# Kernel optimization log

Hardware: AMD Instinct MI355X
Metric: run time of the kernel (lower is better)

Reference implementation:

```python
import jax, jax.numpy as jnp
import numpy as np


def setup_inputs() -> dict:
    key = jax.random.key(0)
    k1, k2, k3, k4 = jax.random.split(key, 4)
    B, T, F, U = 64, 1024, 256, 512
    x = jax.random.normal(k1, (B, T, F), dtype=jnp.float32)
    # small init scale keeps the linear-activation cell state numerically tame
    kernel = jax.random.normal(k2, (F, 4 * U), dtype=jnp.float32) * 0.05
    recurrent_kernel = jax.random.normal(k3, (U, 4 * U), dtype=jnp.float32) * 0.05
    bias = jax.random.normal(k4, (4 * U,), dtype=jnp.float32) * 0.05
    return {"x": x, "kernel": kernel, "recurrent_kernel": recurrent_kernel, "bias": bias}


def reference(x, kernel, recurrent_kernel, bias):
    # Keras LSTM with activation=None (linear candidate / linear output),
    # recurrent_activation=sigmoid, gate order [i, f, c, o]; then external tanh.
    B, T, F = x.shape
    U = recurrent_kernel.shape[0]
    # precompute input projections for all timesteps: [T, B, 4U]
    xz = jnp.einsum('btf,fg->tbg', x, kernel) + bias

    def step(carry, xz_t):
        h, c = carry
        z = xz_t + h @ recurrent_kernel  # [B, 4U]
        i, f, g, o = jnp.split(z, 4, axis=-1)
        i = jax.nn.sigmoid(i)
        f = jax.nn.sigmoid(f)
        o = jax.nn.sigmoid(o)
        c = f * c + i * g          # candidate activation is linear (None)
        h = o * c                  # output activation is linear (None)
        return (h, c), h

    h0 = jnp.zeros((B, U), dtype=x.dtype)
    c0 = jnp.zeros((B, U), dtype=x.dtype)
    (_, _), hs = jax.lax.scan(step, (h0, c0), xz)  # hs: [T, B, U]
    seq = jnp.swapaxes(hs, 0, 1)  # [B, T, U] (return_sequences=True)
    return jnp.tanh(seq)          # external activation applied post-hoc
```

## Files before the change

### kernel.cpp

```cpp
#include <hip/hip_runtime.h>
#include <stdint.h>


#define Tt   1024
#define Uu   512
#define G4U  2048
#define NWG  256
#define NTHR 128
#define TAGSTRIDE 16

#define WF_ELEMS (2 * 24 * 64 * 8)
#define WF_BYTES (WF_ELEMS * 2)
#define ZB_PLANE (16 * 17)
#define ZB_HALF  (4 * ZB_PLANE)
#define SMEM_BYTES (WF_BYTES + 2 * ZB_HALF * 4)

typedef short  bf16x8 __attribute__((ext_vector_type(8)));
typedef float  f32x4  __attribute__((ext_vector_type(4)));
typedef int    int4v  __attribute__((ext_vector_type(4)));
typedef unsigned int u32;

__device__ __forceinline__ unsigned short f2bf(float f) {
  u32 u = __builtin_bit_cast(u32, f);
  u += 0x7fffu + ((u >> 16) & 1u);
  return (unsigned short)(u >> 16);
}
__device__ __forceinline__ u32 umin32(u32 a, u32 b) { return a < b ? a : b; }

__device__ __forceinline__ int4v ld16_ag(const u32* p) {
  int4v r;
  asm volatile("global_load_dwordx4 %0, %1, off sc1"
               : "=v"(r) : "v"(p) : "memory");
  return r;
}
__device__ __forceinline__ int4v ld16_nc(const float* p) {
  int4v r;
  asm volatile("global_load_dwordx4 %0, %1, off"
               : "=v"(r) : "v"(p) : "memory");
  return r;
}
__device__ __forceinline__ void store4_ag(u32* p, u32 v) {
  asm volatile("global_store_dword %0, %1, off sc1"
               :: "v"(p), "v"(v) : "memory");
}

__device__ __forceinline__ float sigf(float z) {
  return __builtin_amdgcn_rcpf(1.f + __expf(-z));
}
__device__ __forceinline__ float tanh_fast(float v) {
  const float e = __expf(-2.f * fabsf(v));
  const float r = (1.f - e) * __builtin_amdgcn_rcpf(1.f + e);
  return copysignf(r, v);
}

extern "C" __global__ void __launch_bounds__(NTHR, 1)
lstm_persistent(const float* __restrict__ x,
                const float* __restrict__ Wk,
                const float* __restrict__ Rk,
                const float* __restrict__ bias,
                float* __restrict__ out,
                u32* __restrict__ hbuf,
                u32* __restrict__ tags)
{
  extern __shared__ char smem[];
  unsigned short* wf   = (unsigned short*)smem;
  float*          zbuf = (float*)(smem + WF_BYTES);

  const int bid = blockIdx.x;
  const int tid = threadIdx.x;
  const int w   = tid >> 6;
  const int l   = tid & 63;
  const int g   = bid & 3;
  const int m   = bid >> 2;

  for (int i = tid; i < WF_ELEMS; i += NTHR) {
    const int j    = i & 7;
    const int lane = (i >> 3) & 63;
    const int kt   = (i >> 9) % 24;
    const int nt   = (i >> 9) / 24;
    const int k    = kt * 32 + ((lane >> 4) << 3) + j;
    const int n    = nt * 16 + (lane & 15);
    const int zc   = (n >> 3) * Uu + m * 8 + (n & 7);
    const float v  = (k < 256) ? Wk[(size_t)k * G4U + zc]
                               : Rk[(size_t)(k - 256) * G4U + zc];
    wf[i] = f2bf(v);
  }
  __syncthreads();

  bf16x8 wfx[4][2];
  #pragma unroll
  for (int q = 0; q < 4; ++q)
    #pragma unroll
    for (int nt = 0; nt < 2; ++nt)
      wfx[q][nt] = *(const bf16x8*)(wf + (((nt * 24) + (2 * q + w)) * 64 + l) * 8);

  const int row_c = tid >> 3;
  const int uu    = tid & 7;
  const int b_out = g * 16 + row_c;
  const int u_out = m * 8 + uu;
  float breg[4];
  #pragma unroll
  for (int gg = 0; gg < 4; ++gg) breg[gg] = bias[gg * Uu + u_out];
  float creg = 0.f;

  const int b_ld = g * 16 + (l & 15);
  const int kq   = (l >> 4) * 8;
  const u32* tagp = tags + ((size_t)g * 64 + l) * TAGSTRIDE;

  int4v xv[4][2];
  {
    const float* xp0 = x + ((size_t)b_ld * Tt + 0) * 256 + kq;
    #pragma unroll
    for (int q = 0; q < 4; ++q) {
      const int kt = 2 * q + w;
      xv[q][0] = ld16_nc(xp0 + kt * 32);
      xv[q][1] = ld16_nc(xp0 + kt * 32 + 4);
    }
  }
  u32 tv = 0;
  if (w == 0)
    asm volatile("global_load_dword %0, %1, off sc1"
                 : "=v"(tv) : "v"(tagp) : "memory");
  asm volatile("s_waitcnt vmcnt(0)" ::: "memory");
  __builtin_amdgcn_sched_barrier(0);

  for (int t = 0; t < Tt; ++t) {
    f32x4 aX0 = {0.f, 0.f, 0.f, 0.f};
    f32x4 aX1 = {0.f, 0.f, 0.f, 0.f};
    #pragma unroll
    for (int q = 0; q < 4; ++q) {
      const f32x4 v0 = __builtin_bit_cast(f32x4, xv[q][0]);
      const f32x4 v1 = __builtin_bit_cast(f32x4, xv[q][1]);
      int r0, r1, r2, r3;
      asm("v_cvt_pk_bf16_f32 %0, %1, %2" : "=v"(r0) : "v"(v0[0]), "v"(v0[1]));
      asm("v_cvt_pk_bf16_f32 %0, %1, %2" : "=v"(r1) : "v"(v0[2]), "v"(v0[3]));
      asm("v_cvt_pk_bf16_f32 %0, %1, %2" : "=v"(r2) : "v"(v1[0]), "v"(v1[1]));
      asm("v_cvt_pk_bf16_f32 %0, %1, %2" : "=v"(r3) : "v"(v1[2]), "v"(v1[3]));
      const int4v ai = {r0, r1, r2, r3};
      const bf16x8 a = __builtin_bit_cast(bf16x8, ai);
      aX0 = __builtin_amdgcn_mfma_f32_16x16x32_bf16(a, wfx[q][0], aX0, 0, 0, 0);
      aX1 = __builtin_amdgcn_mfma_f32_16x16x32_bf16(a, wfx[q][1], aX1, 0, 0, 0);
    }

    if (w == 0) {
      asm volatile("s_waitcnt vmcnt(1)" ::: "memory");
      __builtin_amdgcn_sched_barrier(0);
      while (!__all(tv >= (u32)t)) {
        __builtin_amdgcn_s_sleep(1);
        asm volatile("global_load_dword %0, %1, off sc1\n\ts_waitcnt vmcnt(0)"
                     : "=v"(tv) : "v"(tagp) : "memory");
        __builtin_amdgcn_sched_barrier(0);
      }
    }
    __builtin_amdgcn_s_barrier();
    __builtin_amdgcn_sched_barrier(0);

    const u32* hp = hbuf + ((size_t)(t & 1) * 64 + b_ld) * Uu + kq;
    int4v hf[16];
    #pragma unroll
    for (int q = 0; q < 8; ++q) {
      hf[2 * q]     = ld16_ag(hp + (2 * q + w) * 32);
      hf[2 * q + 1] = ld16_ag(hp + (2 * q + w) * 32 + 4);
    }
    {
      const int tn = (t + 1 < Tt) ? t + 1 : t;
      const float* xpn = x + ((size_t)b_ld * Tt + tn) * 256 + kq;
      #pragma unroll
      for (int q = 0; q < 4; ++q) {
        const int kt = 2 * q + w;
        xv[q][0] = ld16_nc(xpn + kt * 32);
        xv[q][1] = ld16_nc(xpn + kt * 32 + 4);
      }
    }

    asm volatile("s_waitcnt vmcnt(8)" ::: "memory");
    __builtin_amdgcn_sched_barrier(0);
    for (;;) {
      u32 m0 = ~0u, m1 = ~0u, m2 = ~0u, m3 = ~0u;
      #pragma unroll
      for (int q = 0; q < 16; ++q) {
        m0 = umin32(m0, (u32)hf[q][0]);
        m1 = umin32(m1, (u32)hf[q][1]);
        m2 = umin32(m2, (u32)hf[q][2]);
        m3 = umin32(m3, (u32)hf[q][3]);
      }
      const u32 mv = umin32(umin32(m0, m1), umin32(m2, m3));
      if (__all((mv >> 16) == (u32)t)) break;
      __builtin_amdgcn_s_sleep(1);
      #pragma unroll
      for (int q = 0; q < 8; ++q) {
        hf[2 * q]     = ld16_ag(hp + (2 * q + w) * 32);
        hf[2 * q + 1] = ld16_ag(hp + (2 * q + w) * 32 + 4);
      }
      asm volatile("s_waitcnt vmcnt(0)" ::: "memory");
      __builtin_amdgcn_sched_barrier(0);
    }

    f32x4 aH0 = {0.f, 0.f, 0.f, 0.f};
    f32x4 aH1 = {0.f, 0.f, 0.f, 0.f};
    #pragma unroll
    for (int q = 0; q < 8; ++q) {
      const int kt = 8 + 2 * q + w;
      const u32 w0_ = __builtin_amdgcn_perm((u32)hf[2*q][1],   (u32)hf[2*q][0],   0x05040100u);
      const u32 w1_ = __builtin_amdgcn_perm((u32)hf[2*q][3],   (u32)hf[2*q][2],   0x05040100u);
      const u32 w2_ = __builtin_amdgcn_perm((u32)hf[2*q+1][1], (u32)hf[2*q+1][0], 0x05040100u);
      const u32 w3_ = __builtin_amdgcn_perm((u32)hf[2*q+1][3], (u32)hf[2*q+1][2], 0x05040100u);
      const int4v ai = {(int)w0_, (int)w1_, (int)w2_, (int)w3_};
      const bf16x8 a = __builtin_bit_cast(bf16x8, ai);
      const bf16x8 b0 = *(const bf16x8*)(wf + ((0 * 24 + kt) * 64 + l) * 8);
      const bf16x8 b1 = *(const bf16x8*)(wf + ((1 * 24 + kt) * 64 + l) * 8);
      aH0 = __builtin_amdgcn_mfma_f32_16x16x32_bf16(a, b0, aH0, 0, 0, 0);
      aH1 = __builtin_amdgcn_mfma_f32_16x16x32_bf16(a, b1, aH1, 0, 0, 0);
    }

    const f32x4 z0 = aX0 + aH0;
    const f32x4 z1 = aX1 + aH1;

    float* zb = zbuf + (t & 1) * ZB_HALF;
    {
      float* zw = zb + ((w * 2 + 0) * 16 + (l >> 4) * 4) * 17 + (l & 15);
      #pragma unroll
      for (int r = 0; r < 4; ++r) {
        zw[r * 17]           = z0[r];
        zw[r * 17 + 16 * 17] = z1[r];
      }
    }
    __syncthreads();

    float z[4];
    #pragma unroll
    for (int gg = 0; gg < 4; ++gg) {
      const int n  = gg * 8 + uu;
      const int nt = n >> 4, nc = n & 15;
      z[gg] = zb[((0 + nt) * 16 + row_c) * 17 + nc]
            + zb[((2 + nt) * 16 + row_c) * 17 + nc]
            + breg[gg];
    }
    const float ig = sigf(z[0]);
    const float fg = sigf(z[1]);
    const float og = sigf(z[3]);
    const float cc = fg * creg + ig * z[2];
    creg = cc;
    const float hh = og * cc;

    asm volatile("s_waitcnt vmcnt(0)" ::: "memory");
    __builtin_amdgcn_sched_barrier(0);
    const u32 hw = ((u32)(t + 1) << 16) | (u32)f2bf(hh);
    store4_ag(hbuf + ((size_t)((t + 1) & 1) * 64 + b_out) * Uu + u_out, hw);
    __builtin_amdgcn_s_barrier();
    __builtin_amdgcn_sched_barrier(0);
    if (tid == 0)
      store4_ag(tags + ((size_t)g * 64 + m) * TAGSTRIDE, (u32)(t + 1));
    if (w == 0)
      asm volatile("global_load_dword %0, %1, off sc1"
                   : "=v"(tv) : "v"(tagp) : "memory");
    {
      const float ov = tanh_fast(hh);
      float* op = out + ((size_t)b_out * Tt + t) * Uu + u_out;
      asm volatile("global_store_dword %0, %1, off nt"
                   :: "v"(op), "v"(ov) : "memory");
    }
  }
}

extern "C" void kernel_launch(void* const* d_in, const int* in_sizes, int n_in,
                              void* d_out, int out_size, void* d_ws, size_t ws_size,
                              hipStream_t stream) {
  const float* x    = (const float*)d_in[0];
  const float* Wk   = (const float*)d_in[1];
  const float* Rk   = (const float*)d_in[2];
  const float* bias = (const float*)d_in[3];
  float* out = (float*)d_out;
  u32* hbuf = (u32*)d_ws;
  u32* tags = (u32*)((char*)d_ws + (size_t)2 * 64 * Uu * sizeof(u32));

  (void)hipMemsetAsync(d_ws, 0,
                       (size_t)2 * 64 * Uu * sizeof(u32)
                         + (size_t)4 * 64 * TAGSTRIDE * sizeof(u32),
                       stream);

  (void)hipFuncSetAttribute((const void*)lstm_persistent,
                            hipFuncAttributeMaxDynamicSharedMemorySize,
                            SMEM_BYTES);

  hipLaunchKernelGGL(lstm_persistent, dim3(NWG), dim3(NTHR), SMEM_BYTES, stream,
                     x, Wk, Rk, bias, out, hbuf, tags);
}
```

Before: 3.174 ms.

## Speculatively prefetch next-step h before polling tags, drop per-step tag barrier

Instead of waiting on a per-group tag flag and a workgroup barrier before loading the recurrent state, each step now issues the h loads for the next timestep right after publishing its own output. It then validates them via the timestamp embedded in each packed element. Tag polling only happens on the slow path when the speculative data is stale, which removes a serial tag round-trip and a barrier from the critical path. The risk is extra reload traffic when the data is stale, plus reliance on vmcnt ordering: a wait of 17 outstanding operations followed by a wait of 1 with the output store in flight.

```diff
diff --git a/kernel.cpp b/kernel.cpp
--- a/kernel.cpp
+++ b/kernel.cpp
@@ -42,6 +42,12 @@
 __device__ __forceinline__ void store4_ag(u32* p, u32 v) {
   asm volatile("global_store_dword %0, %1, off sc1"
                :: "v"(p), "v"(v) : "memory");
+}
+__device__ __forceinline__ u32 load_tag_wait(const u32* p) {
+  u32 r;
+  asm volatile("global_load_dword %0, %1, off sc1\n\ts_waitcnt vmcnt(0)"
+               : "=v"(r) : "v"(p) : "memory");
+  return r;
 }
 
 __device__ __forceinline__ float sigf(float z) {
@@ -108,6 +114,7 @@
   const u32* tagp = tags + ((size_t)g * 64 + l) * TAGSTRIDE;
 
   int4v xv[4][2];
+  int4v hf[16];
   {
     const float* xp0 = x + ((size_t)b_ld * Tt + 0) * 256 + kq;
     #pragma unroll
@@ -116,15 +123,20 @@
       xv[q][0] = ld16_nc(xp0 + kt * 32);
       xv[q][1] = ld16_nc(xp0 + kt * 32 + 4);
     }
+    const u32* hp0 = hbuf + (size_t)b_ld * Uu + kq;
+    #pragma unroll
+    for (int q = 0; q < 8; ++q) {
+      hf[2 * q]     = ld16_ag(hp0 + (2 * q + w) * 32);
+      hf[2 * q + 1] = ld16_ag(hp0 + (2 * q + w) * 32 + 4);
+    }
   }
-  u32 tv = 0;
-  if (w == 0)
-    asm volatile("global_load_dword %0, %1, off sc1"
-                 : "=v"(tv) : "v"(tagp) : "memory");
   asm volatile("s_waitcnt vmcnt(0)" ::: "memory");
   __builtin_amdgcn_sched_barrier(0);
 
   for (int t = 0; t < Tt; ++t) {
+    asm volatile("s_waitcnt vmcnt(17)" ::: "memory");
+    __builtin_amdgcn_sched_barrier(0);
+
     f32x4 aX0 = {0.f, 0.f, 0.f, 0.f};
     f32x4 aX1 = {0.f, 0.f, 0.f, 0.f};
     #pragma unroll
@@ -142,39 +154,9 @@
       aX1 = __builtin_amdgcn_mfma_f32_16x16x32_bf16(a, wfx[q][1], aX1, 0, 0, 0);
     }
 
-    if (w == 0) {
-      asm volatile("s_waitcnt vmcnt(1)" ::: "memory");
-      __builtin_amdgcn_sched_barrier(0);
-      while (!__all(tv >= (u32)t)) {
-        __builtin_amdgcn_s_sleep(1);
-        asm volatile("global_load_dword %0, %1, off sc1\n\ts_waitcnt vmcnt(0)"
-                     : "=v"(tv) : "v"(tagp) : "memory");
-        __builtin_amdgcn_sched_barrier(0);
-      }
-    }
-    __builtin_amdgcn_s_barrier();
-    __builtin_amdgcn_sched_barrier(0);
-
+    asm volatile("s_waitcnt vmcnt(1)" ::: "memory");
+    __builtin_amdgcn_sched_barrier(0);
     const u32* hp = hbuf + ((size_t)(t & 1) * 64 + b_ld) * Uu + kq;
-    int4v hf[16];
-    #pragma unroll
-    for (int q = 0; q < 8; ++q) {
-      hf[2 * q]     = ld16_ag(hp + (2 * q + w) * 32);
-      hf[2 * q + 1] = ld16_ag(hp + (2 * q + w) * 32 + 4);
-    }
-    {
-      const int tn = (t + 1 < Tt) ? t + 1 : t;
-      const float* xpn = x + ((size_t)b_ld * Tt + tn) * 256 + kq;
-      #pragma unroll
-      for (int q = 0; q < 4; ++q) {
-        const int kt = 2 * q + w;
-        xv[q][0] = ld16_nc(xpn + kt * 32);
-        xv[q][1] = ld16_nc(xpn + kt * 32 + 4);
-      }
-    }
-
-    asm volatile("s_waitcnt vmcnt(8)" ::: "memory");
-    __builtin_amdgcn_sched_barrier(0);
     for (;;) {
       u32 m0 = ~0u, m1 = ~0u, m2 = ~0u, m3 = ~0u;
       #pragma unroll
@@ -186,7 +168,11 @@
       }
       const u32 mv = umin32(umin32(m0, m1), umin32(m2, m3));
       if (__all((mv >> 16) == (u32)t)) break;
-      __builtin_amdgcn_s_sleep(1);
+      u32 tv;
+      do {
+        __builtin_amdgcn_s_sleep(1);
+        tv = load_tag_wait(tagp);
+      } while (!__all(tv >= (u32)t));
       #pragma unroll
       for (int q = 0; q < 8; ++q) {
         hf[2 * q]     = ld16_ag(hp + (2 * q + w) * 32);
@@ -243,17 +229,30 @@
     creg = cc;
     const float hh = og * cc;
 
-    asm volatile("s_waitcnt vmcnt(0)" ::: "memory");
-    __builtin_amdgcn_sched_barrier(0);
     const u32 hw = ((u32)(t + 1) << 16) | (u32)f2bf(hh);
     store4_ag(hbuf + ((size_t)((t + 1) & 1) * 64 + b_out) * Uu + u_out, hw);
+    asm volatile("s_waitcnt vmcnt(0)" ::: "memory");
+    __builtin_amdgcn_sched_barrier(0);
     __builtin_amdgcn_s_barrier();
     __builtin_amdgcn_sched_barrier(0);
     if (tid == 0)
       store4_ag(tags + ((size_t)g * 64 + m) * TAGSTRIDE, (u32)(t + 1));
-    if (w == 0)
-      asm volatile("global_load_dword %0, %1, off sc1"
-                   : "=v"(tv) : "v"(tagp) : "memory");
+    {
+      const int tn = (t + 1 < Tt) ? t + 1 : t;
+      const float* xpn = x + ((size_t)b_ld * Tt + tn) * 256 + kq;
+      #pragma unroll
+      for (int q = 0; q < 4; ++q) {
+        const int kt = 2 * q + w;
+        xv[q][0] = ld16_nc(xpn + kt * 32);
+        xv[q][1] = ld16_nc(xpn + kt * 32 + 4);
+      }
+      const u32* hpn = hbuf + ((size_t)((t + 1) & 1) * 64 + b_ld) * Uu + kq;
+      #pragma unroll
+      for (int q = 0; q < 8; ++q) {
+        hf[2 * q]     = ld16_ag(hpn + (2 * q + w) * 32);
+        hf[2 * q + 1] = ld16_ag(hpn + (2 * q + w) * 32 + 4);
+      }
+    }
     {
       const float ov = tanh_fast(hh);
       float* op = out + ((size_t)b_out * Tt + t) * Uu + u_out;
```

New measurement: 3.850 ms. 1.21x slower.
